# Optimization experiments

Hardware: AMD Instinct MI355X
Metric: run time of the kernel (lower is better)

## Reference

```python
import jax, jax.numpy as jnp
import numpy as np

B, N, D, E = 2, 50000, 128, 800000
EPS = 1e-5


def layer_norm(x, gamma, beta):
    m = jnp.mean(x, axis=-1, keepdims=True)
    v = jnp.mean((x - m) ** 2, axis=-1, keepdims=True)
    return (x - m) * jax.lax.rsqrt(v + EPS) * gamma + beta


def setup_inputs() -> dict:
    key = jax.random.key(0)
    ks = jax.random.split(key, 8)
    x = jax.random.normal(ks[0], (B, N, D), dtype=jnp.float32)
    edge_src = jax.random.randint(ks[1], (E,), 0, N)
    edge_dst = jax.random.randint(ks[2], (E,), 0, N)
    # degree consistent with edge_dst (in-degree), as a float tensor
    degree = jax.ops.segment_sum(jnp.ones((E,), jnp.float32), edge_dst, num_segments=N)
    # LayerNorm params (torch default init: gamma=1, beta=0)
    sn_g = jnp.ones((D,), jnp.float32); sn_b = jnp.zeros((D,), jnp.float32)
    nn_g = jnp.ones((D,), jnp.float32); nn_b = jnp.zeros((D,), jnp.float32)
    # MLP: Linear(2D, 2D) -> GELU -> Linear(2D, D); stored as [in, out]
    s1 = 1.0 / np.sqrt(2 * D)
    W1 = jax.random.uniform(ks[3], (2 * D, 2 * D), jnp.float32, -s1, s1)
    b1 = jax.random.uniform(ks[4], (2 * D,), jnp.float32, -s1, s1)
    W2 = jax.random.uniform(ks[5], (2 * D, D), jnp.float32, -s1, s1)
    b2 = jax.random.uniform(ks[6], (D,), jnp.float32, -s1, s1)
    return {"x": x, "edge_src": edge_src, "edge_dst": edge_dst, "degree": degree,
            "sn_g": sn_g, "sn_b": sn_b, "nn_g": nn_g, "nn_b": nn_b,
            "W1": W1, "b1": b1, "W2": W2, "b2": b2}


def reference(x, edge_src, edge_dst, degree, sn_g, sn_b, nn_g, nn_b, W1, b1, W2, b2):
    # gather messages from source nodes, scatter-add into destination nodes
    neighbor = jnp.zeros_like(x).at[:, edge_dst, :].add(x[:, edge_src, :])  # [B,N,D]
    neighbor = neighbor / jnp.clip(degree, 1.0)[None, :, None]
    h = jnp.concatenate([layer_norm(x, sn_g, sn_b), layer_norm(neighbor, nn_g, nn_b)], axis=-1)  # [B,N,2D]
    h = jax.nn.gelu(h @ W1 + b1, approximate=False)  # torch nn.GELU default = exact erf
    return x + (h @ W2 + b2)
```

## Files before the change

### kernel.cpp

```cpp
#include <hip/hip_runtime.h>
#include <cstdint>

#define B_ 2
#define N_ 50000
#define D_ 128
#define E_ 800000
#define TOK 100000

typedef __bf16 bf16x8 __attribute__((ext_vector_type(8)));
typedef float f32x4 __attribute__((ext_vector_type(4)));

__device__ __forceinline__ unsigned short f2bf(float f) {
  union { float f; uint32_t u; } v; v.f = f;
  uint32_t u = v.u;
  return (unsigned short)((u + 0x7FFFu + ((u >> 16) & 1u)) >> 16);
}
__device__ __forceinline__ float uasf(uint32_t u) {
  union { uint32_t u; float f; } v; v.u = u; return v.f;
}
__device__ __forceinline__ float fast_gelu(float v) {
  float p = v * (1.5957691f + 0.07135481f * v * v);
  return v * __builtin_amdgcn_rcpf(1.0f + __expf(-p));
}

__global__ __launch_bounds__(256) void prep_k(
    const float* __restrict__ x, const float* __restrict__ W1,
    const float* __restrict__ W2, const int* __restrict__ edst,
    unsigned short* __restrict__ xb, unsigned short* __restrict__ W1t,
    unsigned short* __restrict__ W2t, int* __restrict__ cnt) {
  const int blk = blockIdx.x;
  if (blk < 12500) {
    int q = (blk * 256 + threadIdx.x) * 4;
    int node = q >> 8;
    int rem = q & 255;
    int b = rem >> 7, c = rem & 127;
    float4 v = *(const float4*)(x + (size_t)b * (N_ * D_) + node * 128 + c);
    uint2 p = { (uint32_t)f2bf(v.x) | ((uint32_t)f2bf(v.y) << 16),
                (uint32_t)f2bf(v.z) | ((uint32_t)f2bf(v.w) << 16) };
    *(uint2*)(xb + q) = p;
  } else if (blk < 12884) {
    int t = (blk - 12500) * 256 + threadIdx.x;
    if (t < 65536) {
      int n = t >> 8, k = t & 255;
      int f = (n >> 4) * 8 + (k >> 5);
      int pos = ((n & 15) + ((k >> 3) & 3) * 16) * 8 + (k & 7);
      W1t[f * 512 + pos] = f2bf(W1[k * 256 + n]);
    } else {
      int t2 = t - 65536;
      int n = t2 >> 8, k = t2 & 255;
      int f = (n >> 4) * 8 + (k >> 5);
      int pos = ((n & 15) + ((k >> 3) & 3) * 16) * 8 + (k & 7);
      W2t[f * 512 + pos] = f2bf(W2[k * 128 + n]);
    }
  } else {
    int e = (blk - 12884) * 256 + threadIdx.x;
    if (e < E_) atomicAdd(&cnt[edst[e]], 1);
  }
}

__global__ __launch_bounds__(1024) void scan1_k(const int* __restrict__ cnt,
                                                int* __restrict__ part,
                                                int* __restrict__ bsum) {
  __shared__ int wsum[16], woff[16];
  const int tid = threadIdx.x, lane = tid & 63, wv = tid >> 6;
  int i = blockIdx.x * 1024 + tid;
  int v = (i < N_) ? cnt[i] : 0;
  int s = v;
#pragma unroll
  for (int off = 1; off < 64; off <<= 1) {
    int t = __shfl_up(s, off);
    if (lane >= off) s += t;
  }
  if (lane == 63) wsum[wv] = s;
  __syncthreads();
  if (tid == 0) {
    int a = 0;
#pragma unroll
    for (int w = 0; w < 16; ++w) { woff[w] = a; a += wsum[w]; }
    bsum[blockIdx.x] = a;
  }
  __syncthreads();
  if (i < N_) part[i] = woff[wv] + s - v;
}

__global__ __launch_bounds__(64) void scan2_k(const int* __restrict__ bsum,
                                              int* __restrict__ boff) {
  int lane = threadIdx.x;
  int v = (lane < 49) ? bsum[lane] : 0;
  int s = v;
#pragma unroll
  for (int off = 1; off < 64; off <<= 1) {
    int t = __shfl_up(s, off);
    if (lane >= off) s += t;
  }
  boff[lane] = s - v;
}

__global__ __launch_bounds__(1024) void scan3_k(const int* __restrict__ part,
                                                const int* __restrict__ boff,
                                                int* __restrict__ rs,
                                                int* __restrict__ cursor) {
  int i = blockIdx.x * 1024 + threadIdx.x;
  if (i < N_) {
    int v = part[i] + boff[blockIdx.x];
    rs[i] = v; cursor[i] = v;
  }
  if (i == 0) rs[N_] = E_;
}

__global__ __launch_bounds__(256) void fill_k(const int* __restrict__ esrc,
                                              const int* __restrict__ edst,
                                              int* __restrict__ cursor,
                                              int* __restrict__ sorted_src) {
  int e = blockIdx.x * 256 + threadIdx.x;
  if (e < E_) {
    int pos = atomicAdd(&cursor[edst[e]], 1);
    sorted_src[pos] = esrc[e];
  }
}

__global__ __launch_bounds__(256) void gather_ln_k(
    const unsigned short* __restrict__ xb,
    const int* __restrict__ rs, const int* __restrict__ ss,
    const float* __restrict__ sn_g, const float* __restrict__ sn_b,
    const float* __restrict__ nn_g, const float* __restrict__ nn_b,
    unsigned short* __restrict__ h) {
  const int node = blockIdx.x * 4 + (threadIdx.x >> 6);
  const int lane = threadIdx.x & 63;
  const int g = lane >> 5;
  const int l32 = lane & 31;
  const int r0 = rs[node], r1 = rs[node + 1];
  const unsigned short* xrow = xb + l32 * 8;
  float acc[8] = {0.f, 0.f, 0.f, 0.f, 0.f, 0.f, 0.f, 0.f};
  for (int e = r0; e < r1; e += 16) {
    int idx[8];
#pragma unroll
    for (int j = 0; j < 8; ++j) {
      int ej = e + 2 * j + g;
      idx[j] = ss[(ej < r1) ? ej : r0];
    }
    uint4 v[8];
#pragma unroll
    for (int j = 0; j < 8; ++j)
      v[j] = *(const uint4*)(xrow + (size_t)idx[j] * 256);
#pragma unroll
    for (int j = 0; j < 8; ++j) {
      if (e + 2 * j + g < r1) {
        acc[0] += uasf(v[j].x << 16); acc[1] += uasf(v[j].x & 0xffff0000u);
        acc[2] += uasf(v[j].y << 16); acc[3] += uasf(v[j].y & 0xffff0000u);
        acc[4] += uasf(v[j].z << 16); acc[5] += uasf(v[j].z & 0xffff0000u);
        acc[6] += uasf(v[j].w << 16); acc[7] += uasf(v[j].w & 0xffff0000u);
      }
    }
  }
#pragma unroll
  for (int k = 0; k < 8; ++k) acc[k] += __shfl_xor(acc[k], 32);
  const float invd = 1.0f / fmaxf((float)(r1 - r0), 1.0f);
  float nb[8];
#pragma unroll
  for (int k = 0; k < 8; ++k) nb[k] = acc[k] * invd;
  uint4 xq = *(const uint4*)(xrow + (size_t)node * 256);
  float xv[8];
  xv[0] = uasf(xq.x << 16); xv[1] = uasf(xq.x & 0xffff0000u);
  xv[2] = uasf(xq.y << 16); xv[3] = uasf(xq.y & 0xffff0000u);
  xv[4] = uasf(xq.z << 16); xv[5] = uasf(xq.z & 0xffff0000u);
  xv[6] = uasf(xq.w << 16); xv[7] = uasf(xq.w & 0xffff0000u);
  float sx = 0.f, sxx = 0.f, sn = 0.f, snn = 0.f;
#pragma unroll
  for (int k = 0; k < 8; ++k) {
    sx += xv[k]; sxx += xv[k] * xv[k];
    sn += nb[k]; snn += nb[k] * nb[k];
  }
#pragma unroll
  for (int off = 1; off < 16; off <<= 1) {
    sx  += __shfl_xor(sx, off);  sxx += __shfl_xor(sxx, off);
    sn  += __shfl_xor(sn, off);  snn += __shfl_xor(snn, off);
  }
  const float r = 1.0f / 128.0f;
  float mx = sx * r, vx = fmaxf(sxx * r - mx * mx, 0.f);
  float mn = sn * r, vn = fmaxf(snn * r - mn * mn, 0.f);
  float rx = rsqrtf(vx + 1e-5f), rn = rsqrtf(vn + 1e-5f);
  const int c = (l32 & 15) * 8;
  const float* gp = g ? nn_g : sn_g;
  const float* bp = g ? nn_b : sn_b;
  float4 g0 = *(const float4*)(gp + c), g1 = *(const float4*)(gp + c + 4);
  float4 b0 = *(const float4*)(bp + c), b1v = *(const float4*)(bp + c + 4);
  float gw[8] = {g0.x, g0.y, g0.z, g0.w, g1.x, g1.y, g1.z, g1.w};
  float bw[8] = {b0.x, b0.y, b0.z, b0.w, b1v.x, b1v.y, b1v.z, b1v.w};
  float mu = g ? mn : mx;
  float rs_ = g ? rn : rx;
  float o[8];
#pragma unroll
  for (int k = 0; k < 8; ++k) {
    float s = g ? nb[k] : xv[k];
    o[k] = (s - mu) * rs_ * gw[k] + bw[k];
  }
  uint4 po;
  po.x = (uint32_t)f2bf(o[0]) | ((uint32_t)f2bf(o[1]) << 16);
  po.y = (uint32_t)f2bf(o[2]) | ((uint32_t)f2bf(o[3]) << 16);
  po.z = (uint32_t)f2bf(o[4]) | ((uint32_t)f2bf(o[5]) << 16);
  po.w = (uint32_t)f2bf(o[6]) | ((uint32_t)f2bf(o[7]) << 16);
  unsigned short* hr = h + ((size_t)(l32 >> 4) * N_ + node) * 256 + g * 128 + c;
  *(uint4*)hr = po;
}

__global__ __launch_bounds__(512, 2) void fused_mlp_k(
    const unsigned short* __restrict__ A,
    const unsigned short* __restrict__ W1t,
    const unsigned short* __restrict__ W2t,
    const float* __restrict__ b1,
    const float* __restrict__ b2,
    const float* __restrict__ resid,
    float* __restrict__ outp, int M) {
  __shared__ unsigned short As[128 * 256];
  __shared__ unsigned short Hc[128 * 64];
  const int tid = threadIdx.x;
  const int wave = tid >> 6, lane = tid & 63;
  const int wr = wave >> 1;
  const int wc = wave & 1;
  const int quad = lane >> 4, l15 = lane & 15;
  const int m0 = blockIdx.x * 128;
  {
    uint4 v[8];
#pragma unroll
    for (int it = 0; it < 8; ++it) {
      int id = it * 512 + tid;
      int r = id >> 5, c16 = id & 31;
      int gm = m0 + r;
      uint4 va = {0u, 0u, 0u, 0u};
      if (gm < M) va = *(const uint4*)(A + (size_t)gm * 256 + c16 * 8);
      v[it] = va;
    }
#pragma unroll
    for (int it = 0; it < 8; ++it) {
      int id = it * 512 + tid;
      int r = id >> 5, c16 = id & 31;
      *(uint4*)(&As[r * 256 + (c16 ^ (r & 7)) * 8]) = v[it];
    }
  }
  f32x4 acc2[2][4] = {};
  __syncthreads();
  for (int nc = 0; nc < 4; ++nc) {
    f32x4 acc1[2][2] = {};
#pragma unroll
    for (int kc = 0; kc < 256; kc += 32) {
      bf16x8 a[2], b[2];
#pragma unroll
      for (int i = 0; i < 2; ++i) {
        int row = wr * 32 + i * 16 + l15;
        a[i] = *(const bf16x8*)(&As[row * 256 + ((kc + quad * 8) ^ ((row & 7) << 3))]);
      }
#pragma unroll
      for (int i = 0; i < 2; ++i) {
        int ftile = (nc * 4 + wc * 2 + i) * 8 + (kc >> 5);
        b[i] = *(const bf16x8*)(W1t + ftile * 512 + lane * 8);
      }
#pragma unroll
      for (int mi = 0; mi < 2; ++mi)
#pragma unroll
        for (int ni = 0; ni < 2; ++ni)
          acc1[mi][ni] = __builtin_amdgcn_mfma_f32_16x16x32_bf16(a[mi], b[ni], acc1[mi][ni], 0, 0, 0);
    }
    __syncthreads();
#pragma unroll
    for (int mi = 0; mi < 2; ++mi)
#pragma unroll
      for (int ni = 0; ni < 2; ++ni) {
        int col = wc * 32 + ni * 16 + l15;
        float bv = b1[nc * 64 + col];
#pragma unroll
        for (int rr = 0; rr < 4; ++rr) {
          int row = wr * 32 + mi * 16 + quad * 4 + rr;
          Hc[row * 64 + (col ^ ((row & 7) << 3))] = f2bf(fast_gelu(acc1[mi][ni][rr] + bv));
        }
      }
    __syncthreads();
#pragma unroll
    for (int kc = 0; kc < 64; kc += 32) {
      bf16x8 a[2], b[4];
#pragma unroll
      for (int i = 0; i < 2; ++i) {
        int row = wr * 32 + i * 16 + l15;
        a[i] = *(const bf16x8*)(&Hc[row * 64 + ((kc + quad * 8) ^ ((row & 7) << 3))]);
      }
#pragma unroll
      for (int i = 0; i < 4; ++i) {
        int ftile = (wc * 4 + i) * 8 + nc * 2 + (kc >> 5);
        b[i] = *(const bf16x8*)(W2t + ftile * 512 + lane * 8);
      }
#pragma unroll
      for (int mi = 0; mi < 2; ++mi)
#pragma unroll
        for (int ni = 0; ni < 4; ++ni)
          acc2[mi][ni] = __builtin_amdgcn_mfma_f32_16x16x32_bf16(a[mi], b[ni], acc2[mi][ni], 0, 0, 0);
    }
  }
#pragma unroll
  for (int mi = 0; mi < 2; ++mi)
#pragma unroll
    for (int ni = 0; ni < 4; ++ni) {
      int col = wc * 64 + ni * 16 + l15;
      float bv = b2[col];
#pragma unroll
      for (int rr = 0; rr < 4; ++rr) {
        int row = m0 + wr * 32 + mi * 16 + quad * 4 + rr;
        if (row < M) {
          float v = acc2[mi][ni][rr] + bv + resid[(size_t)row * 128 + col];
          outp[(size_t)row * 128 + col] = v;
        }
      }
    }
}

extern "C" void kernel_launch(void* const* d_in, const int* in_sizes, int n_in,
                              void* d_out, int out_size, void* d_ws, size_t ws_size,
                              hipStream_t stream) {
  const float* x    = (const float*)d_in[0];
  const int* esrc   = (const int*)d_in[1];
  const int* edst   = (const int*)d_in[2];
  const float* sn_g = (const float*)d_in[4];
  const float* sn_b = (const float*)d_in[5];
  const float* nn_g = (const float*)d_in[6];
  const float* nn_b = (const float*)d_in[7];
  const float* W1   = (const float*)d_in[8];
  const float* b1   = (const float*)d_in[9];
  const float* W2   = (const float*)d_in[10];
  const float* b2   = (const float*)d_in[11];

  char* ws = (char*)d_ws;
  const size_t H_BYTES = (size_t)TOK * 256 * 2;
  unsigned short* h = (unsigned short*)ws;
  char* csr = ws + H_BYTES;
  int* cnt        = (int*)(csr);
  int* part       = (int*)(csr + 200000);
  int* rs         = (int*)(csr + 400000);
  int* cursor     = (int*)(csr + 600016);
  int* bsum       = (int*)(csr + 800016);
  int* boff       = (int*)(csr + 800224);
  int* sorted_src = (int*)(csr + 800512);
  unsigned short* xb = (unsigned short*)(csr + 4194304);
  unsigned short* W1t = (unsigned short*)(ws + 2 * H_BYTES);
  unsigned short* W2t = W1t + 65536;

  hipMemsetAsync(cnt, 0, (size_t)N_ * sizeof(int), stream);
  prep_k<<<16009, 256, 0, stream>>>(x, W1, W2, edst, xb, W1t, W2t, cnt);
  scan1_k<<<49, 1024, 0, stream>>>(cnt, part, bsum);
  scan2_k<<<1, 64, 0, stream>>>(bsum, boff);
  scan3_k<<<49, 1024, 0, stream>>>(part, boff, rs, cursor);
  fill_k<<<(E_ + 255) / 256, 256, 0, stream>>>(esrc, edst, cursor, sorted_src);
  gather_ln_k<<<N_ / 4, 256, 0, stream>>>(xb, rs, sorted_src,
                                          sn_g, sn_b, nn_g, nn_b, h);
  fused_mlp_k<<<(TOK + 127) / 128, 512, 0, stream>>>(h, W1t, W2t, b1, b2,
                                                     x, (float*)d_out, TOK);
}
```

Measured before the change: 324.7 us.

## Make MLP waves independent with direct global A loads; merge scan into one kernel

```diff
diff --git a/kernel.cpp b/kernel.cpp
--- a/kernel.cpp
+++ b/kernel.cpp
@@ -58,54 +58,56 @@
   }
 }
 
-__global__ __launch_bounds__(1024) void scan1_k(const int* __restrict__ cnt,
-                                                int* __restrict__ part,
-                                                int* __restrict__ bsum) {
-  __shared__ int wsum[16], woff[16];
+__global__ __launch_bounds__(1024) void scan_all_k(const int* __restrict__ cnt,
+                                                   int* __restrict__ rs,
+                                                   int* __restrict__ cursor) {
+  __shared__ int wsum[16], woff[16], carry[2];
   const int tid = threadIdx.x, lane = tid & 63, wv = tid >> 6;
-  int i = blockIdx.x * 1024 + tid;
-  int v = (i < N_) ? cnt[i] : 0;
-  int s = v;
-#pragma unroll
-  for (int off = 1; off < 64; off <<= 1) {
-    int t = __shfl_up(s, off);
-    if (lane >= off) s += t;
-  }
-  if (lane == 63) wsum[wv] = s;
+  if (tid == 0) carry[0] = 0;
+  int p = 0;
   __syncthreads();
-  if (tid == 0) {
-    int a = 0;
-#pragma unroll
-    for (int w = 0; w < 16; ++w) { woff[w] = a; a += wsum[w]; }
-    bsum[blockIdx.x] = a;
-  }
-  __syncthreads();
-  if (i < N_) part[i] = woff[wv] + s - v;
-}
-
-__global__ __launch_bounds__(64) void scan2_k(const int* __restrict__ bsum,
-                                              int* __restrict__ boff) {
-  int lane = threadIdx.x;
-  int v = (lane < 49) ? bsum[lane] : 0;
-  int s = v;
-#pragma unroll
-  for (int off = 1; off < 64; off <<= 1) {
-    int t = __shfl_up(s, off);
-    if (lane >= off) s += t;
-  }
-  boff[lane] = s - v;
-}
-
-__global__ __launch_bounds__(1024) void scan3_k(const int* __restrict__ part,
-                                                const int* __restrict__ boff,
-                                                int* __restrict__ rs,
-                                                int* __restrict__ cursor) {
-  int i = blockIdx.x * 1024 + threadIdx.x;
-  if (i < N_) {
-    int v = part[i] + boff[blockIdx.x];
-    rs[i] = v; cursor[i] = v;
-  }
-  if (i == 0) rs[N_] = E_;
+  for (int base = 0; base < N_; base += 4096) {
+    int i = base + tid * 4;
+    int4 v = {0, 0, 0, 0};
+    if (i + 3 < N_) {
+      v = *(const int4*)(cnt + i);
+    } else {
+      if (i     < N_) v.x = cnt[i];
+      if (i + 1 < N_) v.y = cnt[i + 1];
+      if (i + 2 < N_) v.z = cnt[i + 2];
+      if (i + 3 < N_) v.w = cnt[i + 3];
+    }
+    int s4 = v.x + v.y + v.z + v.w;
+    int s = s4;
+#pragma unroll
+    for (int off = 1; off < 64; off <<= 1) {
+      int t = __shfl_up(s, off);
+      if (lane >= off) s += t;
+    }
+    if (lane == 63) wsum[wv] = s;
+    __syncthreads();
+    if (tid == 0) {
+      int a = 0;
+#pragma unroll
+      for (int w = 0; w < 16; ++w) { woff[w] = a; a += wsum[w]; }
+      carry[p ^ 1] = carry[p] + a;
+    }
+    __syncthreads();
+    int pre = carry[p] + woff[wv] + (s - s4);
+    int e0 = pre, e1 = pre + v.x, e2 = e1 + v.y, e3 = e2 + v.z;
+    if (i + 3 < N_) {
+      int4 w0 = {e0, e1, e2, e3};
+      *(int4*)(rs + i) = w0;
+      *(int4*)(cursor + i) = w0;
+    } else {
+      if (i     < N_) { rs[i]     = e0; cursor[i]     = e0; }
+      if (i + 1 < N_) { rs[i + 1] = e1; cursor[i + 1] = e1; }
+      if (i + 2 < N_) { rs[i + 2] = e2; cursor[i + 2] = e2; }
+      if (i + 3 < N_) { rs[i + 3] = e3; cursor[i + 3] = e3; }
+    }
+    p ^= 1;
+  }
+  if (tid == 0) rs[N_] = E_;
 }
 
 __global__ __launch_bounds__(256) void fill_k(const int* __restrict__ esrc,
@@ -204,7 +206,7 @@
   *(uint4*)hr = po;
 }
 
-__global__ __launch_bounds__(512, 2) void fused_mlp_k(
+__global__ __launch_bounds__(256, 4) void fused_mlp_k(
     const unsigned short* __restrict__ A,
     const unsigned short* __restrict__ W1t,
     const unsigned short* __restrict__ W2t,
@@ -212,47 +214,25 @@
     const float* __restrict__ b2,
     const float* __restrict__ resid,
     float* __restrict__ outp, int M) {
-  __shared__ unsigned short As[128 * 256];
-  __shared__ unsigned short Hc[128 * 64];
+  __shared__ unsigned short Hc[4][32][32];
   const int tid = threadIdx.x;
-  const int wave = tid >> 6, lane = tid & 63;
-  const int wr = wave >> 1;
-  const int wc = wave & 1;
+  const int wv = tid >> 6, lane = tid & 63;
   const int quad = lane >> 4, l15 = lane & 15;
-  const int m0 = blockIdx.x * 128;
-  {
-    uint4 v[8];
-#pragma unroll
-    for (int it = 0; it < 8; ++it) {
-      int id = it * 512 + tid;
-      int r = id >> 5, c16 = id & 31;
-      int gm = m0 + r;
-      uint4 va = {0u, 0u, 0u, 0u};
-      if (gm < M) va = *(const uint4*)(A + (size_t)gm * 256 + c16 * 8);
-      v[it] = va;
-    }
-#pragma unroll
-    for (int it = 0; it < 8; ++it) {
-      int id = it * 512 + tid;
-      int r = id >> 5, c16 = id & 31;
-      *(uint4*)(&As[r * 256 + (c16 ^ (r & 7)) * 8]) = v[it];
-    }
-  }
-  f32x4 acc2[2][4] = {};
-  __syncthreads();
-  for (int nc = 0; nc < 4; ++nc) {
+  const int rowbase = blockIdx.x * 128 + wv * 32;
+  f32x4 acc2[2][8] = {};
+  for (int nc = 0; nc < 8; ++nc) {
     f32x4 acc1[2][2] = {};
 #pragma unroll
     for (int kc = 0; kc < 256; kc += 32) {
       bf16x8 a[2], b[2];
 #pragma unroll
       for (int i = 0; i < 2; ++i) {
-        int row = wr * 32 + i * 16 + l15;
-        a[i] = *(const bf16x8*)(&As[row * 256 + ((kc + quad * 8) ^ ((row & 7) << 3))]);
+        int row = rowbase + i * 16 + l15;
+        a[i] = *(const bf16x8*)(A + (size_t)row * 256 + kc + quad * 8);
       }
 #pragma unroll
       for (int i = 0; i < 2; ++i) {
-        int ftile = (nc * 4 + wc * 2 + i) * 8 + (kc >> 5);
+        int ftile = (nc * 2 + i) * 8 + (kc >> 5);
         b[i] = *(const bf16x8*)(W1t + ftile * 512 + lane * 8);
       }
 #pragma unroll
@@ -261,49 +241,46 @@
         for (int ni = 0; ni < 2; ++ni)
           acc1[mi][ni] = __builtin_amdgcn_mfma_f32_16x16x32_bf16(a[mi], b[ni], acc1[mi][ni], 0, 0, 0);
     }
-    __syncthreads();
+    asm volatile("s_waitcnt lgkmcnt(0)" ::: "memory");
 #pragma unroll
     for (int mi = 0; mi < 2; ++mi)
 #pragma unroll
       for (int ni = 0; ni < 2; ++ni) {
-        int col = wc * 32 + ni * 16 + l15;
-        float bv = b1[nc * 64 + col];
+        int col = ni * 16 + l15;
+        float bv = b1[nc * 32 + col];
 #pragma unroll
         for (int rr = 0; rr < 4; ++rr) {
-          int row = wr * 32 + mi * 16 + quad * 4 + rr;
-          Hc[row * 64 + (col ^ ((row & 7) << 3))] = f2bf(fast_gelu(acc1[mi][ni][rr] + bv));
+          int row = mi * 16 + quad * 4 + rr;
+          Hc[wv][row][col ^ ((row & 3) << 3)] = f2bf(fast_gelu(acc1[mi][ni][rr] + bv));
         }
       }
-    __syncthreads();
-#pragma unroll
-    for (int kc = 0; kc < 64; kc += 32) {
-      bf16x8 a[2], b[4];
-#pragma unroll
-      for (int i = 0; i < 2; ++i) {
-        int row = wr * 32 + i * 16 + l15;
-        a[i] = *(const bf16x8*)(&Hc[row * 64 + ((kc + quad * 8) ^ ((row & 7) << 3))]);
-      }
-#pragma unroll
-      for (int i = 0; i < 4; ++i) {
-        int ftile = (wc * 4 + i) * 8 + nc * 2 + (kc >> 5);
-        b[i] = *(const bf16x8*)(W2t + ftile * 512 + lane * 8);
-      }
-#pragma unroll
-      for (int mi = 0; mi < 2; ++mi)
-#pragma unroll
-        for (int ni = 0; ni < 4; ++ni)
-          acc2[mi][ni] = __builtin_amdgcn_mfma_f32_16x16x32_bf16(a[mi], b[ni], acc2[mi][ni], 0, 0, 0);
-    }
+    asm volatile("s_waitcnt lgkmcnt(0)" ::: "memory");
+    bf16x8 a2[2], bw2[8];
+#pragma unroll
+    for (int i = 0; i < 2; ++i) {
+      int row = i * 16 + l15;
+      a2[i] = *(const bf16x8*)(&Hc[wv][row][(quad * 8) ^ ((row & 3) << 3)]);
+    }
+#pragma unroll
+    for (int i = 0; i < 8; ++i) {
+      int ftile = i * 8 + nc;
+      bw2[i] = *(const bf16x8*)(W2t + ftile * 512 + lane * 8);
+    }
+#pragma unroll
+    for (int mi = 0; mi < 2; ++mi)
+#pragma unroll
+      for (int ni = 0; ni < 8; ++ni)
+        acc2[mi][ni] = __builtin_amdgcn_mfma_f32_16x16x32_bf16(a2[mi], bw2[ni], acc2[mi][ni], 0, 0, 0);
   }
 #pragma unroll
   for (int mi = 0; mi < 2; ++mi)
 #pragma unroll
-    for (int ni = 0; ni < 4; ++ni) {
-      int col = wc * 64 + ni * 16 + l15;
+    for (int ni = 0; ni < 8; ++ni) {
+      int col = ni * 16 + l15;
       float bv = b2[col];
 #pragma unroll
       for (int rr = 0; rr < 4; ++rr) {
-        int row = m0 + wr * 32 + mi * 16 + quad * 4 + rr;
+        int row = rowbase + mi * 16 + quad * 4 + rr;
         if (row < M) {
           float v = acc2[mi][ni][rr] + bv + resid[(size_t)row * 128 + col];
           outp[(size_t)row * 128 + col] = v;
@@ -332,11 +309,8 @@
   unsigned short* h = (unsigned short*)ws;
   char* csr = ws + H_BYTES;
   int* cnt        = (int*)(csr);
-  int* part       = (int*)(csr + 200000);
   int* rs         = (int*)(csr + 400000);
   int* cursor     = (int*)(csr + 600016);
-  int* bsum       = (int*)(csr + 800016);
-  int* boff       = (int*)(csr + 800224);
   int* sorted_src = (int*)(csr + 800512);
   unsigned short* xb = (unsigned short*)(csr + 4194304);
   unsigned short* W1t = (unsigned short*)(ws + 2 * H_BYTES);
@@ -344,12 +318,10 @@
 
   hipMemsetAsync(cnt, 0, (size_t)N_ * sizeof(int), stream);
   prep_k<<<16009, 256, 0, stream>>>(x, W1, W2, edst, xb, W1t, W2t, cnt);
-  scan1_k<<<49, 1024, 0, stream>>>(cnt, part, bsum);
-  scan2_k<<<1, 64, 0, stream>>>(bsum, boff);
-  scan3_k<<<49, 1024, 0, stream>>>(part, boff, rs, cursor);
+  scan_all_k<<<1, 1024, 0, stream>>>(cnt, rs, cursor);
   fill_k<<<(E_ + 255) / 256, 256, 0, stream>>>(esrc, edst, cursor, sorted_src);
   gather_ln_k<<<N_ / 4, 256, 0, stream>>>(xb, rs, sorted_src,
                                           sn_g, sn_b, nn_g, nn_b, h);
-  fused_mlp_k<<<(TOK + 127) / 128, 512, 0, stream>>>(h, W1t, W2t, b1, b2,
+  fused_mlp_k<<<(TOK + 127) / 128, 256, 0, stream>>>(h, W1t, W2t, b1, b2,
                                                      x, (float*)d_out, TOK);
 }
```

Measured after the change: 383.2 us. 1.18x slower.
